# Kernel optimization log

Measured on AMD Instinct MI355X. Metric: run time of the kernel, lower is better.

## Reference

```python
import jax, jax.numpy as jnp
import numpy as np

B, S, H = 32, 1024, 512
NEG = -1e10

def setup_inputs() -> dict:
    key = jax.random.key(0)
    k1, k2, k3, k4, k5, k6 = jax.random.split(key, 6)
    return {
        "hidden": jax.random.normal(k1, (B, H), jnp.float32),
        "encoder_outputs": jax.random.normal(k2, (B, S, 2 * H), jnp.float32),
        "mask": jax.random.randint(k3, (B, S), 0, 2, jnp.int32),
        "W_attn": jax.random.normal(k4, (3 * H, H), jnp.float32) * (1.0 / np.sqrt(3 * H)),
        "b_attn": jax.random.normal(k5, (H,), jnp.float32) * 0.01,
        "W_v": jax.random.normal(k6, (H,), jnp.float32) * (1.0 / np.sqrt(H)),
    }

def reference(hidden, encoder_outputs, mask, W_attn, b_attn, W_v):
    # Split the concat-matmul: cat([h, enc]) @ W_attn == h @ W_h + enc @ W_e
    W_h, W_e = W_attn[:H], W_attn[H:]            # [H,H], [2H,H]
    proj_h = hidden @ W_h                        # [B, H]
    proj_e = jnp.einsum('bse,eh->bsh', encoder_outputs, W_e)  # [B, S, H]
    energy = jnp.tanh(proj_h[:, None, :] + proj_e + b_attn)   # [B, S, H]
    scores = jnp.einsum('bsh,h->bs', energy, W_v)             # [B, S]
    scores = jnp.where(mask == 0, NEG, scores)
    attn_w = jax.nn.softmax(scores, axis=1)                   # [B, S]
    context = jnp.einsum('bs,bse->be', attn_w, encoder_outputs)  # [B, 2H]
    return context, attn_w
```

## Files before the change

kernel.cpp:

```cpp
#include <hip/hip_runtime.h>
#include <hip/hip_bf16.h>
#include <math.h>

#define NB 32
#define NS 1024
#define NH 512
#define NE 1024
#define NEGV -1e10f

typedef _Float16 f16x8 __attribute__((ext_vector_type(8)));
typedef _Float16 f16x4 __attribute__((ext_vector_type(4)));
typedef float f32x4 __attribute__((ext_vector_type(4)));

__device__ __forceinline__ float fast_tanh(float x) {
  float t = __expf(2.f * x);
  return (t - 1.f) * __builtin_amdgcn_rcpf(t + 1.f);
}

__global__ __launch_bounds__(256) void proj_h_kernel(
    const float* __restrict__ hidden, const float* __restrict__ W_attn,
    const float* __restrict__ b_attn, float* __restrict__ c) {
  int b = blockIdx.x >> 1;
  int h = ((blockIdx.x & 1) << 8) + threadIdx.x;
  __shared__ float hid[NH];
  for (int e = threadIdx.x; e < NH; e += 256) hid[e] = hidden[b * NH + e];
  __syncthreads();
  float acc = b_attn[h];
#pragma unroll 8
  for (int e = 0; e < NH; ++e) acc = fmaf(hid[e], W_attn[(size_t)e * NH + h], acc);
  c[b * NH + h] = acc;
}

__global__ __launch_bounds__(256) void prep_We_kernel(
    const float* __restrict__ W_attn, _Float16* __restrict__ Bp) {
  int ks = blockIdx.x;
  int t = threadIdx.x;
#pragma unroll
  for (int p = 0; p < 8; ++p) {
    int f = (p << 8) + t;
    int ws = f >> 8;
    int nj = (f >> 6) & 3;
    int lane = f & 63;
    int col = (ws << 6) + (nj << 4) + (lane & 15);
    int kb = (ks << 5) + ((lane >> 4) << 3);
    f16x8 h;
#pragma unroll
    for (int j = 0; j < 8; ++j)
      h[j] = (_Float16)W_attn[(size_t)(NH + kb + j) * NH + col];
    *(f16x8*)((char*)Bp + (size_t)(((ks << 3) + ws) << 12) + (nj << 10) + (lane << 4)) = h;
  }
}

__global__ __launch_bounds__(512) void score_kernel(
    const float* __restrict__ enc, const _Float16* __restrict__ Bp,
    const float* __restrict__ c, const float* __restrict__ Wv,
    float* __restrict__ spart) {
  __shared__ _Float16 Afp16[64 * 1024];
  const int tid = threadIdx.x;
  const int lane = tid & 63;
  const int wid = tid >> 6;
  const int r15 = lane & 15;
  const int id = blockIdx.x;
  const int mt = ((id & 7) << 6) + (id >> 3);
  const int b = mt >> 4;
  const int s0 = (mt & 15) << 6;
  const float* encb = enc + ((size_t)b * NS + s0) * NE;
  const char* Bbase = (const char*)Bp + ((size_t)wid << 12);

#pragma unroll 4
  for (int p = 0; p < 32; ++p) {
    int f = (p << 9) + tid;
    int row = f >> 8;
    int kq = f & 255;
    float4 v = *(const float4*)(encb + ((size_t)row << 10) + (kq << 2));
    f16x4 h;
    h[0] = (_Float16)v.x; h[1] = (_Float16)v.y;
    h[2] = (_Float16)v.z; h[3] = (_Float16)v.w;
    int off = (row << 11) + (kq << 3);
    off ^= (row & 7) << 4;
    *(f16x4*)((char*)Afp16 + off) = h;
  }
  __syncthreads();

  f32x4 acc[4][4];
#pragma unroll
  for (int i = 0; i < 4; ++i)
#pragma unroll
    for (int j = 0; j < 4; ++j) acc[i][j] = (f32x4)0.f;

#define BLOAD(ARR, KS)                                                           \
  _Pragma("unroll") for (int nj = 0; nj < 4; ++nj)                               \
      ARR[nj] = *(const f16x8*)(Bbase + ((size_t)(KS) << 15) +                   \
                                (nj << 10) + (lane << 4));

#define COMPUTE(KS, ARR)                                                         \
  {                                                                              \
    f16x8 af[4];                                                                 \
    _Pragma("unroll") for (int mi = 0; mi < 4; ++mi) {                           \
      int row = (mi << 4) + r15;                                                 \
      int off = (row << 11) + ((KS) << 6) + ((lane >> 4) << 4);                  \
      off ^= (row & 7) << 4;                                                     \
      af[mi] = *(const f16x8*)((const char*)Afp16 + off);                        \
    }                                                                            \
    _Pragma("unroll") for (int mi = 0; mi < 4; ++mi)                             \
      _Pragma("unroll") for (int nj = 0; nj < 4; ++nj)                           \
        acc[mi][nj] = __builtin_amdgcn_mfma_f32_16x16x32_f16(af[mi], ARR[nj],    \
                                                             acc[mi][nj], 0, 0, 0); \
  }

  f16x8 bfE[4], bfO[4];
  BLOAD(bfE, 0);
  for (int ks = 0; ks < 32; ks += 2) {
    BLOAD(bfO, ks + 1);
    COMPUTE(ks, bfE);
    if (ks < 30) BLOAD(bfE, ks + 2);
    COMPUTE(ks + 1, bfO);
  }
#undef BLOAD
#undef COMPUTE

  float sr[4][4];
#pragma unroll
  for (int i = 0; i < 4; ++i)
#pragma unroll
    for (int r = 0; r < 4; ++r) sr[i][r] = 0.f;
#pragma unroll
  for (int nj = 0; nj < 4; ++nj) {
    int hcol = (wid << 6) + (nj << 4) + r15;
    float wvj = Wv[hcol];
    float cvj = c[b * NH + hcol];
#pragma unroll
    for (int mi = 0; mi < 4; ++mi)
#pragma unroll
      for (int r = 0; r < 4; ++r)
        sr[mi][r] += wvj * fast_tanh(acc[mi][nj][r] + cvj);
  }
#pragma unroll
  for (int off = 1; off < 16; off <<= 1)
#pragma unroll
    for (int mi = 0; mi < 4; ++mi)
#pragma unroll
      for (int r = 0; r < 4; ++r) sr[mi][r] += __shfl_xor(sr[mi][r], off, 64);
  if (r15 == 0) {
    float* dst = spart + (size_t)wid * NB * NS + b * NS + s0;
#pragma unroll
    for (int mi = 0; mi < 4; ++mi)
#pragma unroll
      for (int r = 0; r < 4; ++r)
        dst[(mi << 4) + ((lane >> 4) << 2) + r] = sr[mi][r];
  }
}

__global__ __launch_bounds__(256) void softmax_kernel(
    const float* __restrict__ spart, const int* __restrict__ mask,
    float* __restrict__ attn) {
  int b = blockIdx.x, tid = threadIdx.x;
  __shared__ float red[8];
  float v[4];
  float mx = -INFINITY;
#pragma unroll
  for (int j = 0; j < 4; ++j) {
    int s = tid + (j << 8);
    float x = 0.f;
#pragma unroll
    for (int p = 0; p < 8; ++p) x += spart[(size_t)p * NB * NS + b * NS + s];
    v[j] = (mask[b * NS + s] == 0) ? NEGV : x;
    mx = fmaxf(mx, v[j]);
  }
#pragma unroll
  for (int off = 32; off >= 1; off >>= 1) mx = fmaxf(mx, __shfl_xor(mx, off, 64));
  if ((tid & 63) == 0) red[tid >> 6] = mx;
  __syncthreads();
  mx = fmaxf(fmaxf(red[0], red[1]), fmaxf(red[2], red[3]));
  float sum = 0.f;
#pragma unroll
  for (int j = 0; j < 4; ++j) {
    v[j] = __expf(v[j] - mx);
    sum += v[j];
  }
#pragma unroll
  for (int off = 32; off >= 1; off >>= 1) sum += __shfl_xor(sum, off, 64);
  __syncthreads();
  if ((tid & 63) == 0) red[4 + (tid >> 6)] = sum;
  __syncthreads();
  float inv = 1.f / (red[4] + red[5] + red[6] + red[7]);
#pragma unroll
  for (int j = 0; j < 4; ++j) attn[b * NS + tid + (j << 8)] = v[j] * inv;
}

__global__ __launch_bounds__(256) void ctx_partial_kernel(
    const float* __restrict__ enc, const float* __restrict__ attn,
    float* __restrict__ partial) {
  int ch = blockIdx.x;
  int b = blockIdx.y;
  int tid = threadIdx.x;
  __shared__ float w[64];
  if (tid < 64) w[tid] = attn[b * NS + (ch << 6) + tid];
  __syncthreads();
  const float* encb = enc + ((size_t)b * NS + (ch << 6)) * NE;
  float4 acc = make_float4(0.f, 0.f, 0.f, 0.f);
  int e = tid << 2;
  for (int s = 0; s < 64; ++s) {
    float4 x = *(const float4*)(encb + (size_t)s * NE + e);
    float ws_ = w[s];
    acc.x = fmaf(ws_, x.x, acc.x);
    acc.y = fmaf(ws_, x.y, acc.y);
    acc.z = fmaf(ws_, x.z, acc.z);
    acc.w = fmaf(ws_, x.w, acc.w);
  }
  *(float4*)(partial + ((size_t)(b * 16 + ch)) * NE + e) = acc;
}

__global__ __launch_bounds__(256) void ctx_reduce_kernel(
    const float* __restrict__ partial, float* __restrict__ ctx) {
  int b = blockIdx.x;
  int e = threadIdx.x << 2;
  float4 acc = make_float4(0.f, 0.f, 0.f, 0.f);
  for (int ch = 0; ch < 16; ++ch) {
    float4 x = *(const float4*)(partial + ((size_t)(b * 16 + ch)) * NE + e);
    acc.x += x.x;
    acc.y += x.y;
    acc.z += x.z;
    acc.w += x.w;
  }
  *(float4*)(ctx + (size_t)b * NE + e) = acc;
}

extern "C" void kernel_launch(void* const* d_in, const int* in_sizes, int n_in,
                              void* d_out, int out_size, void* d_ws, size_t ws_size,
                              hipStream_t stream) {
  const float* hidden = (const float*)d_in[0];
  const float* enc = (const float*)d_in[1];
  const int* mask = (const int*)d_in[2];
  const float* W_attn = (const float*)d_in[3];
  const float* b_attn = (const float*)d_in[4];
  const float* W_v = (const float*)d_in[5];

  float* ctx = (float*)d_out;
  float* attn = ctx + NB * NS;

  char* ws = (char*)d_ws;
  float* c = (float*)ws;
  float* spart = (float*)(ws + 65536);
  float* partial = (float*)(ws + 65536 + 1048576);
  _Float16* Bp = (_Float16*)(ws + 65536 + 1048576 + 2097152);

  proj_h_kernel<<<64, 256, 0, stream>>>(hidden, W_attn, b_attn, c);
  prep_We_kernel<<<32, 256, 0, stream>>>(W_attn, Bp);
  score_kernel<<<512, 512, 0, stream>>>(enc, Bp, c, W_v, spart);
  softmax_kernel<<<NB, 256, 0, stream>>>(spart, mask, attn);
  ctx_partial_kernel<<<dim3(16, NB), 256, 0, stream>>>(enc, attn, partial);
  ctx_reduce_kernel<<<NB, 256, 0, stream>>>(partial, ctx);
}
```

Baseline: 106.7 us.

## Split encoder tile staging into two K halves overlapped with MFMA compute

The score kernel now stages the 64x1024 encoder tile into LDS in two K-halves. The first half is loaded up front, and the second half's global loads and fp16 conversion are interleaved with the MFMA loop over the first half. The B-fragment register prefetch also goes from double to quadruple buffering. The aim is to hide global-load latency behind compute instead of serialising the full tile load before any MFMA work, at the cost of more registers and a more complex schedule.

```diff
diff --git a/kernel.cpp b/kernel.cpp
--- a/kernel.cpp
+++ b/kernel.cpp
@@ -64,41 +64,47 @@
   const int mt = ((id & 7) << 6) + (id >> 3);
   const int b = mt >> 4;
   const int s0 = (mt & 15) << 6;
-  const float* encb = enc + ((size_t)b * NS + s0) * NE;
+  const char* encB = (const char*)(enc + ((size_t)b * NS + s0) * NE);
   const char* Bbase = (const char*)Bp + ((size_t)wid << 12);
 
-#pragma unroll 4
-  for (int p = 0; p < 32; ++p) {
-    int f = (p << 9) + tid;
-    int row = f >> 8;
-    int kq = f & 255;
-    float4 v = *(const float4*)(encb + ((size_t)row << 10) + (kq << 2));
-    f16x4 h;
-    h[0] = (_Float16)v.x; h[1] = (_Float16)v.y;
-    h[2] = (_Float16)v.z; h[3] = (_Float16)v.w;
-    int off = (row << 11) + (kq << 3);
-    off ^= (row & 7) << 4;
-    *(f16x4*)((char*)Afp16 + off) = h;
-  }
-  __syncthreads();
-
   f32x4 acc[4][4];
 #pragma unroll
   for (int i = 0; i < 4; ++i)
 #pragma unroll
     for (int j = 0; j < 4; ++j) acc[i][j] = (f32x4)0.f;
+
+#define LOADB(V, H, LB)                                                          \
+  _Pragma("unroll") for (int p = 0; p < 4; ++p) {                                \
+    int f = ((((LB) << 2) + p) << 9) + tid;                                      \
+    int row = f >> 7;                                                            \
+    int kq = f & 127;                                                            \
+    V[p] = *(const float4*)(encB + (size_t)row * 4096 + ((H) << 11) + (kq << 4));\
+  }
+
+#define WRITEB(V, H, LB)                                                         \
+  _Pragma("unroll") for (int p = 0; p < 4; ++p) {                                \
+    int f = ((((LB) << 2) + p) << 9) + tid;                                      \
+    int row = f >> 7;                                                            \
+    int kq = f & 127;                                                            \
+    f16x4 h4;                                                                    \
+    h4[0] = (_Float16)V[p].x; h4[1] = (_Float16)V[p].y;                          \
+    h4[2] = (_Float16)V[p].z; h4[3] = (_Float16)V[p].w;                          \
+    int off = ((H) << 16) + (row << 10) + (kq << 3);                             \
+    off ^= (row & 7) << 4;                                                       \
+    *(f16x4*)((char*)Afp16 + off) = h4;                                          \
+  }
 
 #define BLOAD(ARR, KS)                                                           \
   _Pragma("unroll") for (int nj = 0; nj < 4; ++nj)                               \
       ARR[nj] = *(const f16x8*)(Bbase + ((size_t)(KS) << 15) +                   \
                                 (nj << 10) + (lane << 4));
 
-#define COMPUTE(KS, ARR)                                                         \
+#define COMPUTE(H, KSL, ARR)                                                     \
   {                                                                              \
     f16x8 af[4];                                                                 \
     _Pragma("unroll") for (int mi = 0; mi < 4; ++mi) {                           \
       int row = (mi << 4) + r15;                                                 \
-      int off = (row << 11) + ((KS) << 6) + ((lane >> 4) << 4);                  \
+      int off = ((H) << 16) + (row << 10) + ((KSL) << 6) + ((lane >> 4) << 4);   \
       off ^= (row & 7) << 4;                                                     \
       af[mi] = *(const f16x8*)((const char*)Afp16 + off);                        \
     }                                                                            \
@@ -108,14 +114,50 @@
                                                              acc[mi][nj], 0, 0, 0); \
   }
 
-  f16x8 bfE[4], bfO[4];
-  BLOAD(bfE, 0);
-  for (int ks = 0; ks < 32; ks += 2) {
-    BLOAD(bfO, ks + 1);
-    COMPUTE(ks, bfE);
-    if (ks < 30) BLOAD(bfE, ks + 2);
-    COMPUTE(ks + 1, bfO);
-  }
+  {
+    float4 vA[4], vB[4];
+    LOADB(vA, 0, 0); LOADB(vB, 0, 1);
+    WRITEB(vA, 0, 0); LOADB(vA, 0, 2);
+    WRITEB(vB, 0, 1); LOADB(vB, 0, 3);
+    WRITEB(vA, 0, 2); WRITEB(vB, 0, 3);
+  }
+  __syncthreads();
+
+  f16x8 S0[4], S1[4], S2[4], S3[4];
+  BLOAD(S0, 0); BLOAD(S1, 1); BLOAD(S2, 2);
+
+  float4 vS[4];
+  for (int g = 0; g < 4; ++g) {
+    int s = g << 2;
+    BLOAD(S3, s + 3);
+    LOADB(vS, 1, g);
+    COMPUTE(0, s + 0, S0);
+    BLOAD(S0, s + 4);
+    COMPUTE(0, s + 1, S1);
+    BLOAD(S1, s + 5);
+    COMPUTE(0, s + 2, S2);
+    BLOAD(S2, s + 6);
+    WRITEB(vS, 1, g);
+    COMPUTE(0, s + 3, S3);
+  }
+  __syncthreads();
+  for (int g = 0; g < 4; ++g) {
+    int s = 16 + (g << 2);
+    int k0 = s + 3;
+    int k1 = s + 4 > 31 ? 31 : s + 4;
+    int k2 = s + 5 > 31 ? 31 : s + 5;
+    int k3 = s + 6 > 31 ? 31 : s + 6;
+    BLOAD(S3, k0);
+    COMPUTE(1, (g << 2) + 0, S0);
+    BLOAD(S0, k1);
+    COMPUTE(1, (g << 2) + 1, S1);
+    BLOAD(S1, k2);
+    COMPUTE(1, (g << 2) + 2, S2);
+    BLOAD(S2, k3);
+    COMPUTE(1, (g << 2) + 3, S3);
+  }
+#undef LOADB
+#undef WRITEB
 #undef BLOAD
 #undef COMPUTE
 
```

Measured after the change: 105.9 us. About the same (-0.7%).
